# Kernel tuning notes

Measured on AMD Instinct MI355X. Metric: run time of the kernel, lower is better.

Reference implementation:

```python
import jax, jax.numpy as jnp
import numpy as np

N_TOKENS = 32768
DIM = 2048
N_EXPERTS = 64
TOP_K = 8
N_GROUP = 8
TOPK_GROUP = 4
ROUTE_SCALE = 2.5
EPS = 1e-20


def setup_inputs() -> dict:
    key = jax.random.key(0)
    k1, k2 = jax.random.split(key)
    hidden_states = jax.random.normal(k1, (N_TOKENS, DIM), dtype=jnp.float32)
    weight = jax.random.normal(k2, (N_EXPERTS, DIM), dtype=jnp.float32) * 0.02
    e_score_correction_bias = jnp.zeros((N_EXPERTS,), dtype=jnp.float32)
    return {"hidden_states": hidden_states, "weight": weight,
            "e_score_correction_bias": e_score_correction_bias}


def reference(hidden_states, weight, e_score_correction_bias):
    # router logits in fp32: [N, E]
    logits = jnp.einsum('nd,ed->ne', hidden_states.astype(jnp.float32),
                        weight.astype(jnp.float32))
    scores = jax.nn.sigmoid(logits)  # score_func == 'sigmoid'

    # --- top-k index selection (no-grad path in torch) ---
    sfc = scores + e_score_correction_bias[None, :]  # [N, E]
    per_group = N_EXPERTS // N_GROUP
    # group score = sum of top-2 scores within each group: [N, G]
    grouped = sfc.reshape(-1, N_GROUP, per_group)
    group_scores = jax.lax.top_k(grouped, 2)[0].sum(axis=-1)
    # pick top `TOPK_GROUP` groups
    _, group_idx = jax.lax.top_k(group_scores, TOPK_GROUP)  # [N, topk_group]
    n = group_scores.shape[0]
    group_mask = jnp.zeros_like(group_scores).at[
        jnp.arange(n)[:, None], group_idx].set(1.0)  # [N, G]
    score_mask = jnp.repeat(group_mask, per_group, axis=1)  # [N, E]
    masked_scores = jnp.where(score_mask > 0, sfc, 0.0)
    _, topk_indices = jax.lax.top_k(masked_scores, TOP_K)  # [N, top_k]

    # gather weights from *unbiased* scores, normalize, scale
    topk_weights = jnp.take_along_axis(scores, topk_indices, axis=1)
    denom = topk_weights.sum(axis=-1, keepdims=True) + EPS
    topk_weights = topk_weights / denom * ROUTE_SCALE
    return topk_indices, topk_weights
```

## Files before the change

### kernel.cpp

```cpp
#include <hip/hip_runtime.h>
#include <math.h>

#define NT 32768
#define DIM 2048
#define NE 64
#define RSCALE 2.5f
#define REPS 1e-20f
#define KC 32
#define NCH (DIM / KC)
#define TOK 32

#define HL_BUF 6144
#define WL_OFF 12288
#define WL_BUF 12288
#define BS_OFF 36864
#define ARENA 37120

typedef const __attribute__((address_space(1))) void GV;
typedef __attribute__((address_space(3))) void LV;
typedef __attribute__((ext_vector_type(8))) short short8x;
typedef __attribute__((ext_vector_type(4))) float f32x4;
typedef __attribute__((ext_vector_type(4))) unsigned int uint4x;

__device__ __align__(16) char WImg[NCH][3 * 4096];

#define PACKHI(odd, even) __builtin_amdgcn_perm((odd), (even), 0x07060302u)

__device__ __forceinline__ void decomp4(f32x4 x, unsigned int o[6]) {
    unsigned int u0 = __float_as_uint(x.x), u1 = __float_as_uint(x.y);
    unsigned int u2 = __float_as_uint(x.z), u3 = __float_as_uint(x.w);
    o[0] = PACKHI(u1, u0); o[1] = PACKHI(u3, u2);
    float r0 = x.x - __uint_as_float(u0 & 0xffff0000u);
    float r1 = x.y - __uint_as_float(u1 & 0xffff0000u);
    float r2 = x.z - __uint_as_float(u2 & 0xffff0000u);
    float r3 = x.w - __uint_as_float(u3 & 0xffff0000u);
    unsigned int v0 = __float_as_uint(r0), v1 = __float_as_uint(r1);
    unsigned int v2 = __float_as_uint(r2), v3 = __float_as_uint(r3);
    o[2] = PACKHI(v1, v0); o[3] = PACKHI(v3, v2);
    float s0 = r0 - __uint_as_float(v0 & 0xffff0000u);
    float s1 = r1 - __uint_as_float(v1 & 0xffff0000u);
    float s2 = r2 - __uint_as_float(v2 & 0xffff0000u);
    float s3 = r3 - __uint_as_float(v3 & 0xffff0000u);
    o[4] = PACKHI(__float_as_uint(s1), __float_as_uint(s0));
    o[5] = PACKHI(__float_as_uint(s3), __float_as_uint(s2));
}

__device__ __forceinline__ void decomp8(f32x4 a, f32x4 b,
                                        short8x* f0, short8x* f1, short8x* f2) {
    unsigned int oa[6], ob[6];
    decomp4(a, oa); decomp4(b, ob);
    uint4x t0 = {oa[0], oa[1], ob[0], ob[1]};
    uint4x t1 = {oa[2], oa[3], ob[2], ob[3]};
    uint4x t2 = {oa[4], oa[5], ob[4], ob[5]};
    *f0 = __builtin_bit_cast(short8x, t0);
    *f1 = __builtin_bit_cast(short8x, t1);
    *f2 = __builtin_bit_cast(short8x, t2);
}

__global__ void prep_w_kernel(const float* __restrict__ W) {
    const int ch = blockIdx.x;
    const int tid = threadIdx.x;
    const int srow = tid >> 2;
    const int sq   = tid & 3;
    const float* src = W + (size_t)srow * DIM + ch * KC + sq * 8;
    f32x4 lo = *(const f32x4*)src;
    f32x4 hi = *(const f32x4*)(src + 4);
    short8x f0, f1, f2;
    decomp8(lo, hi, &f0, &f1, &f2);
    const int soff = srow * 64 + ((sq ^ ((srow >> 1) & 3)) << 4);
    *(short8x*)&WImg[ch][0 * 4096 + soff] = f0;
    *(short8x*)&WImg[ch][1 * 4096 + soff] = f1;
    *(short8x*)&WImg[ch][2 * 4096 + soff] = f2;
}

#define STAGE_ISSUE(HA, HB, KOFF) do { \
    if (hact) { \
        HA = *(const f32x4*)(hgsrc + (KOFF)); \
        HB = *(const f32x4*)(hgsrc + (KOFF) + 4); \
    } \
} while (0)

#define STAGE_WRITE_H(HA, HB, PN) do { \
    if (hact) { \
        short8x f0_, f1_, f2_; \
        decomp8(HA, HB, &f0_, &f1_, &f2_); \
        *(short8x*)(arena + (PN) * HL_BUF + 0 * 2048 + soff) = f0_; \
        *(short8x*)(arena + (PN) * HL_BUF + 1 * 2048 + soff) = f1_; \
        *(short8x*)(arena + (PN) * HL_BUF + 2 * 2048 + soff) = f2_; \
    } \
} while (0)

#define WSTAGE(CHN, PN) do { \
    const char* ws_ = WImg[(CHN)]; \
    __builtin_amdgcn_global_load_lds((GV*)(ws_ + 0 * 4096 + wgofs), \
        (LV*)(arena + WL_OFF + (PN) * WL_BUF + 0 * 4096 + wlofs), 16, 0, 0); \
    __builtin_amdgcn_global_load_lds((GV*)(ws_ + 1 * 4096 + wgofs), \
        (LV*)(arena + WL_OFF + (PN) * WL_BUF + 1 * 4096 + wlofs), 16, 0, 0); \
    __builtin_amdgcn_global_load_lds((GV*)(ws_ + 2 * 4096 + wgofs), \
        (LV*)(arena + WL_OFF + (PN) * WL_BUF + 2 * 4096 + wlofs), 16, 0, 0); \
} while (0)

#define COMPUTE(P) do { \
    const char* hb = arena + (P) * HL_BUF; \
    const char* wb = arena + WL_OFF + (P) * WL_BUF; \
    short8x a0, a1, a2; \
    { const int t_ = wr * 16 + l15; \
      const int ro_ = t_ * 64 + ((g ^ ((t_ >> 1) & 3)) << 4); \
      a0 = *(const short8x*)(hb + 0 * 2048 + ro_); \
      a1 = *(const short8x*)(hb + 1 * 2048 + ro_); \
      a2 = *(const short8x*)(hb + 2 * 2048 + ro_); } \
    _Pragma("unroll") \
    for (int et = 0; et < 2; ++et) { \
        const int e_ = wc * 32 + et * 16 + l15; \
        const int ro_ = e_ * 64 + ((g ^ ((e_ >> 1) & 3)) << 4); \
        short8x b0 = *(const short8x*)(wb + 0 * 4096 + ro_); \
        short8x b1 = *(const short8x*)(wb + 1 * 4096 + ro_); \
        short8x b2 = *(const short8x*)(wb + 2 * 4096 + ro_); \
        Cm[et] = __builtin_amdgcn_mfma_f32_16x16x32_bf16(a0, b0, Cm[et], 0, 0, 0); \
        Cc[et] = __builtin_amdgcn_mfma_f32_16x16x32_bf16(a1, b0, Cc[et], 0, 0, 0); \
        Cc[et] = __builtin_amdgcn_mfma_f32_16x16x32_bf16(a2, b0, Cc[et], 0, 0, 0); \
        Cc[et] = __builtin_amdgcn_mfma_f32_16x16x32_bf16(a0, b1, Cc[et], 0, 0, 0); \
        Cc[et] = __builtin_amdgcn_mfma_f32_16x16x32_bf16(a1, b1, Cc[et], 0, 0, 0); \
        Cc[et] = __builtin_amdgcn_mfma_f32_16x16x32_bf16(a0, b2, Cc[et], 0, 0, 0); \
    } \
} while (0)

#define DRAIN do { \
    _Pragma("unroll") \
    for (int et = 0; et < 2; ++et) { \
        _Pragma("unroll") \
        for (int r = 0; r < 4; ++r) \
            md[et][r] += (double)Cm[et][r] + (double)Cc[et][r]; \
        Cm[et] = (f32x4)0.0f; Cc[et] = (f32x4)0.0f; \
    } \
} while (0)

__global__ __launch_bounds__(256, 4) void router_kernel(
    const float* __restrict__ H,
    const float* __restrict__ B,
    float* __restrict__ out)
{
    __shared__ __align__(16) char arena[ARENA];
    float* bsf = (float*)(arena + BS_OFF);
    float* scf = (float*)(arena);

    const int tid  = threadIdx.x;
    const int lane = tid & 63;
    const int w    = __builtin_amdgcn_readfirstlane(tid >> 6);
    const int l15  = lane & 15, g = lane >> 4;
    const size_t tb = (size_t)blockIdx.x * TOK;

    if (tid < NE) bsf[tid] = B[tid];

    const bool hact = tid < 128;
    const int srow = tid >> 2;
    const int sq   = tid & 3;
    const float* hgsrc = H + (tb + (size_t)(hact ? srow : 0)) * DIM + sq * 8;
    const int soff = srow * 64 + ((sq ^ ((srow >> 1) & 3)) << 4);

    const int wgofs = tid * 16;
    const int wlofs = w * 1024;

    const int wr = w & 1, wc = w >> 1;

    f32x4 Cm[2], Cc[2];
    double md[2][4];
    #pragma unroll
    for (int et = 0; et < 2; ++et) {
        Cm[et] = (f32x4)0.0f; Cc[et] = (f32x4)0.0f;
        #pragma unroll
        for (int r = 0; r < 4; ++r) md[et][r] = 0.0;
    }

    f32x4 hA0, hA1, hB0, hB1;

    WSTAGE(0, 0);
    STAGE_ISSUE(hA0, hA1, 0);
    STAGE_WRITE_H(hA0, hA1, 0);
    STAGE_ISSUE(hB0, hB1, KC);
    __syncthreads();

    for (int chb = 0; chb < NCH; chb += 2) {
        WSTAGE(chb + 1, 1);
        if (chb + 2 < NCH) STAGE_ISSUE(hA0, hA1, (chb + 2) * KC);
        COMPUTE(0);
        STAGE_WRITE_H(hB0, hB1, 1);
        __syncthreads();

        if (chb + 2 < NCH) {
            WSTAGE(chb + 2, 0);
            STAGE_ISSUE(hB0, hB1, (chb + 3 < NCH) ? (chb + 3) * KC : (chb + 2) * KC);
        }
        COMPUTE(1);
        if (chb + 2 < NCH) STAGE_WRITE_H(hA0, hA1, 0);
        if (((chb + 1) & 7) == 7) DRAIN;
        __syncthreads();
    }

    #pragma unroll
    for (int et = 0; et < 2; ++et)
        #pragma unroll
        for (int r = 0; r < 4; ++r) {
            float logit = (float)md[et][r];
            float s = 1.0f / (1.0f + expf(-logit));
            int t = wr * 16 + g * 4 + r;
            int e = wc * 32 + et * 16 + l15;
            scf[t * 65 + e] = s;
        }
    __syncthreads();

    if ((tid & 7) == 0) {
        const int t = tid >> 3;
        const float* sc = &scf[t * 65];
        float gs[8];
        #pragma unroll
        for (int gg = 0; gg < 8; ++gg) {
            float m1 = -1e30f, m2 = -1e30f;
            #pragma unroll
            for (int j = 0; j < 8; ++j) {
                float v = sc[gg * 8 + j] + bsf[gg * 8 + j];
                if (v > m1) { m2 = m1; m1 = v; }
                else if (v > m2) { m2 = v; }
            }
            gs[gg] = m1 + m2;
        }
        unsigned gmask = 0;
        for (int i = 0; i < 4; ++i) {
            float best = -1e30f; int bg = 0;
            for (int gg = 0; gg < 8; ++gg)
                if (!((gmask >> gg) & 1u) && gs[gg] > best) { best = gs[gg]; bg = gg; }
            gmask |= 1u << bg;
        }
        unsigned long long picked = 0ull;
        int   idxs[8];
        float wts[8];
        float wsum = 0.0f;
        for (int i = 0; i < 8; ++i) {
            float best = -1e30f; int bi = 0;
            for (int e = 0; e < 64; ++e) {
                if ((picked >> e) & 1ull) continue;
                float v = ((gmask >> (e >> 3)) & 1u) ? (sc[e] + bsf[e]) : 0.0f;
                if (v > best) { best = v; bi = e; }
            }
            picked |= 1ull << bi;
            idxs[i] = bi;
            wts[i] = sc[bi];
            wsum += sc[bi];
        }
        const float scale = RSCALE / (wsum + REPS);
        const size_t token = tb + t;
        #pragma unroll
        for (int i = 0; i < 8; ++i) {
            out[token * 8 + i] = (float)idxs[i];
            out[(size_t)NT * 8 + token * 8 + i] = wts[i] * scale;
        }
    }
}

extern "C" void kernel_launch(void* const* d_in, const int* in_sizes, int n_in,
                              void* d_out, int out_size, void* d_ws, size_t ws_size,
                              hipStream_t stream) {
    (void)in_sizes; (void)n_in; (void)out_size; (void)d_ws; (void)ws_size;
    const float* H = (const float*)d_in[0];
    const float* W = (const float*)d_in[1];
    const float* B = (const float*)d_in[2];
    float* out = (float*)d_out;
    prep_w_kernel<<<dim3(NCH), dim3(256), 0, stream>>>(W);
    router_kernel<<<dim3(NT / TOK), dim3(256), 0, stream>>>(H, B, out);
}
```

Baseline: 143.3 us.

## Enlarge router tile to 128 tokens, load H directly to registers, stream W in large chunks

Each block now handles 128 tokens with 8 waves. Each wave reads its 16 token rows of H straight into registers and splits them in place, instead of staging H through LDS. W images are DMA'd into LDS in 48KB half-windows covering 4 K-chunks each, double-buffered, so each wave reuses all 64 experts against its tokens and there are fewer barriers. This removes the H LDS round trip and repeated W traffic across small blocks. In exchange it uses about 98KB of LDS at one block per CU, which cuts occupancy and latency hiding, and there are only 256 blocks.

```diff
diff --git a/kernel.cpp b/kernel.cpp
--- a/kernel.cpp
+++ b/kernel.cpp
@@ -8,13 +8,12 @@
 #define REPS 1e-20f
 #define KC 32
 #define NCH (DIM / KC)
-#define TOK 32
-
-#define HL_BUF 6144
-#define WL_OFF 12288
-#define WL_BUF 12288
-#define BS_OFF 36864
-#define ARENA 37120
+#define TOK 128
+#define NHW 16
+#define HW_BYTES 49152
+
+#define BS_OFF 98304
+#define ARENA 98560
 
 typedef const __attribute__((address_space(1))) void GV;
 typedef __attribute__((address_space(3))) void LV;
@@ -73,61 +72,49 @@
     *(short8x*)&WImg[ch][2 * 4096 + soff] = f2;
 }
 
-#define STAGE_ISSUE(HA, HB, KOFF) do { \
-    if (hact) { \
-        HA = *(const f32x4*)(hgsrc + (KOFF)); \
-        HB = *(const f32x4*)(hgsrc + (KOFF) + 4); \
+#define DMA(HW_, BUFO) do { \
+    const char* s_ = wimgf + (size_t)(HW_) * HW_BYTES + (tid << 4); \
+    _Pragma("unroll") \
+    for (int r_ = 0; r_ < 6; ++r_) \
+        __builtin_amdgcn_global_load_lds((GV*)(s_ + r_ * 8192), \
+            (LV*)(arena + (BUFO) + r_ * 8192 + wlbase), 16, 0, 0); \
+} while (0)
+
+#define HLOAD(HR, HW_) do { \
+    _Pragma("unroll") \
+    for (int c_ = 0; c_ < 4; ++c_) { \
+        const float* p_ = hsrc + ((HW_) * 4 + c_) * KC; \
+        HR[c_][0] = *(const f32x4*)p_; \
+        HR[c_][1] = *(const f32x4*)(p_ + 4); \
     } \
 } while (0)
 
-#define STAGE_WRITE_H(HA, HB, PN) do { \
-    if (hact) { \
-        short8x f0_, f1_, f2_; \
-        decomp8(HA, HB, &f0_, &f1_, &f2_); \
-        *(short8x*)(arena + (PN) * HL_BUF + 0 * 2048 + soff) = f0_; \
-        *(short8x*)(arena + (PN) * HL_BUF + 1 * 2048 + soff) = f1_; \
-        *(short8x*)(arena + (PN) * HL_BUF + 2 * 2048 + soff) = f2_; \
+#define COMPUTE(BUFO, HR) do { \
+    _Pragma("unroll") \
+    for (int c_ = 0; c_ < 4; ++c_) { \
+        short8x a0, a1, a2; \
+        decomp8(HR[c_][0], HR[c_][1], &a0, &a1, &a2); \
+        const char* cb_ = arena + (BUFO) + c_ * 12288; \
+        _Pragma("unroll") \
+        for (int et = 0; et < 4; ++et) { \
+            const int e_ = et * 16 + l15; \
+            const int ro_ = e_ * 64 + ((g ^ ((e_ >> 1) & 3)) << 4); \
+            short8x b0 = *(const short8x*)(cb_ + 0 * 4096 + ro_); \
+            short8x b1 = *(const short8x*)(cb_ + 1 * 4096 + ro_); \
+            short8x b2 = *(const short8x*)(cb_ + 2 * 4096 + ro_); \
+            Cm[et] = __builtin_amdgcn_mfma_f32_16x16x32_bf16(a0, b0, Cm[et], 0, 0, 0); \
+            Cc[et] = __builtin_amdgcn_mfma_f32_16x16x32_bf16(a1, b0, Cc[et], 0, 0, 0); \
+            Cc[et] = __builtin_amdgcn_mfma_f32_16x16x32_bf16(a2, b0, Cc[et], 0, 0, 0); \
+            Cc[et] = __builtin_amdgcn_mfma_f32_16x16x32_bf16(a0, b1, Cc[et], 0, 0, 0); \
+            Cc[et] = __builtin_amdgcn_mfma_f32_16x16x32_bf16(a1, b1, Cc[et], 0, 0, 0); \
+            Cc[et] = __builtin_amdgcn_mfma_f32_16x16x32_bf16(a0, b2, Cc[et], 0, 0, 0); \
+        } \
     } \
 } while (0)
 
-#define WSTAGE(CHN, PN) do { \
-    const char* ws_ = WImg[(CHN)]; \
-    __builtin_amdgcn_global_load_lds((GV*)(ws_ + 0 * 4096 + wgofs), \
-        (LV*)(arena + WL_OFF + (PN) * WL_BUF + 0 * 4096 + wlofs), 16, 0, 0); \
-    __builtin_amdgcn_global_load_lds((GV*)(ws_ + 1 * 4096 + wgofs), \
-        (LV*)(arena + WL_OFF + (PN) * WL_BUF + 1 * 4096 + wlofs), 16, 0, 0); \
-    __builtin_amdgcn_global_load_lds((GV*)(ws_ + 2 * 4096 + wgofs), \
-        (LV*)(arena + WL_OFF + (PN) * WL_BUF + 2 * 4096 + wlofs), 16, 0, 0); \
-} while (0)
-
-#define COMPUTE(P) do { \
-    const char* hb = arena + (P) * HL_BUF; \
-    const char* wb = arena + WL_OFF + (P) * WL_BUF; \
-    short8x a0, a1, a2; \
-    { const int t_ = wr * 16 + l15; \
-      const int ro_ = t_ * 64 + ((g ^ ((t_ >> 1) & 3)) << 4); \
-      a0 = *(const short8x*)(hb + 0 * 2048 + ro_); \
-      a1 = *(const short8x*)(hb + 1 * 2048 + ro_); \
-      a2 = *(const short8x*)(hb + 2 * 2048 + ro_); } \
-    _Pragma("unroll") \
-    for (int et = 0; et < 2; ++et) { \
-        const int e_ = wc * 32 + et * 16 + l15; \
-        const int ro_ = e_ * 64 + ((g ^ ((e_ >> 1) & 3)) << 4); \
-        short8x b0 = *(const short8x*)(wb + 0 * 4096 + ro_); \
-        short8x b1 = *(const short8x*)(wb + 1 * 4096 + ro_); \
-        short8x b2 = *(const short8x*)(wb + 2 * 4096 + ro_); \
-        Cm[et] = __builtin_amdgcn_mfma_f32_16x16x32_bf16(a0, b0, Cm[et], 0, 0, 0); \
-        Cc[et] = __builtin_amdgcn_mfma_f32_16x16x32_bf16(a1, b0, Cc[et], 0, 0, 0); \
-        Cc[et] = __builtin_amdgcn_mfma_f32_16x16x32_bf16(a2, b0, Cc[et], 0, 0, 0); \
-        Cc[et] = __builtin_amdgcn_mfma_f32_16x16x32_bf16(a0, b1, Cc[et], 0, 0, 0); \
-        Cc[et] = __builtin_amdgcn_mfma_f32_16x16x32_bf16(a1, b1, Cc[et], 0, 0, 0); \
-        Cc[et] = __builtin_amdgcn_mfma_f32_16x16x32_bf16(a0, b2, Cc[et], 0, 0, 0); \
-    } \
-} while (0)
-
 #define DRAIN do { \
     _Pragma("unroll") \
-    for (int et = 0; et < 2; ++et) { \
+    for (int et = 0; et < 4; ++et) { \
         _Pragma("unroll") \
         for (int r = 0; r < 4; ++r) \
             md[et][r] += (double)Cm[et][r] + (double)Cc[et][r]; \
@@ -135,7 +122,7 @@
     } \
 } while (0)
 
-__global__ __launch_bounds__(256, 4) void router_kernel(
+__global__ __launch_bounds__(512, 1) void router_kernel(
     const float* __restrict__ H,
     const float* __restrict__ B,
     float* __restrict__ out)
@@ -149,68 +136,57 @@
     const int w    = __builtin_amdgcn_readfirstlane(tid >> 6);
     const int l15  = lane & 15, g = lane >> 4;
     const size_t tb = (size_t)blockIdx.x * TOK;
+    const char* wimgf = &WImg[0][0];
+    const int wlbase = w * 1024;
 
     if (tid < NE) bsf[tid] = B[tid];
 
-    const bool hact = tid < 128;
-    const int srow = tid >> 2;
-    const int sq   = tid & 3;
-    const float* hgsrc = H + (tb + (size_t)(hact ? srow : 0)) * DIM + sq * 8;
-    const int soff = srow * 64 + ((sq ^ ((srow >> 1) & 3)) << 4);
-
-    const int wgofs = tid * 16;
-    const int wlofs = w * 1024;
-
-    const int wr = w & 1, wc = w >> 1;
-
-    f32x4 Cm[2], Cc[2];
-    double md[2][4];
+    const float* hsrc = H + (tb + (size_t)(w * 16 + l15)) * DIM + g * 8;
+
+    f32x4 Cm[4], Cc[4];
+    double md[4][4];
     #pragma unroll
-    for (int et = 0; et < 2; ++et) {
+    for (int et = 0; et < 4; ++et) {
         Cm[et] = (f32x4)0.0f; Cc[et] = (f32x4)0.0f;
         #pragma unroll
         for (int r = 0; r < 4; ++r) md[et][r] = 0.0;
     }
 
-    f32x4 hA0, hA1, hB0, hB1;
-
-    WSTAGE(0, 0);
-    STAGE_ISSUE(hA0, hA1, 0);
-    STAGE_WRITE_H(hA0, hA1, 0);
-    STAGE_ISSUE(hB0, hB1, KC);
+    f32x4 hA[4][2], hB[4][2];
+
+    DMA(0, 0);
+    HLOAD(hA, 0);
     __syncthreads();
 
-    for (int chb = 0; chb < NCH; chb += 2) {
-        WSTAGE(chb + 1, 1);
-        if (chb + 2 < NCH) STAGE_ISSUE(hA0, hA1, (chb + 2) * KC);
-        COMPUTE(0);
-        STAGE_WRITE_H(hB0, hB1, 1);
+    for (int hw = 0; hw < NHW; hw += 2) {
+        DMA(hw + 1, HW_BYTES);
+        HLOAD(hB, hw + 1);
+        COMPUTE(0, hA);
         __syncthreads();
 
-        if (chb + 2 < NCH) {
-            WSTAGE(chb + 2, 0);
-            STAGE_ISSUE(hB0, hB1, (chb + 3 < NCH) ? (chb + 3) * KC : (chb + 2) * KC);
-        }
-        COMPUTE(1);
-        if (chb + 2 < NCH) STAGE_WRITE_H(hA0, hA1, 0);
-        if (((chb + 1) & 7) == 7) DRAIN;
+        if (hw + 2 < NHW) {
+            DMA(hw + 2, 0);
+            HLOAD(hA, hw + 2);
+        }
+        COMPUTE(HW_BYTES, hB);
+        DRAIN;
         __syncthreads();
     }
 
     #pragma unroll
-    for (int et = 0; et < 2; ++et)
+    for (int et = 0; et < 4; ++et)
         #pragma unroll
         for (int r = 0; r < 4; ++r) {
             float logit = (float)md[et][r];
             float s = 1.0f / (1.0f + expf(-logit));
-            int t = wr * 16 + g * 4 + r;
-            int e = wc * 32 + et * 16 + l15;
+            int t = w * 16 + g * 4 + r;
+            int e = et * 16 + l15;
             scf[t * 65 + e] = s;
         }
     __syncthreads();
 
-    if ((tid & 7) == 0) {
-        const int t = tid >> 3;
+    if ((tid & 3) == 0) {
+        const int t = tid >> 2;
         const float* sc = &scf[t * 65];
         float gs[8];
         #pragma unroll
@@ -266,5 +242,5 @@
     const float* B = (const float*)d_in[2];
     float* out = (float*)d_out;
     prep_w_kernel<<<dim3(NCH), dim3(256), 0, stream>>>(W);
-    router_kernel<<<dim3(NT / TOK), dim3(256), 0, stream>>>(H, B, out);
-}
+    router_kernel<<<dim3(NT / TOK), dim3(512), 0, stream>>>(H, B, out);
+}
```

Result: faster. 130.8 us (-8.7%).
